# Kernel optimization log

Measured on AMD Instinct MI355X. Metric: run time of the kernel, lower is better.

The kernel has to match this reference:

```python
import jax, jax.numpy as jnp
import numpy as np

N_NODES = 100000
N_EDGES = 1600000
D = 64
N_LAYERS = 3
N_GRAPHS = 128
BN_EPS = 1e-5


def setup_inputs() -> dict:
    key = jax.random.key(0)
    k_x, k_e, k_b, k_w = jax.random.split(key, 4)
    x = jax.random.normal(k_x, (N_NODES, D), dtype=jnp.float32)
    edge_index = jax.random.randint(k_e, (2, N_EDGES), 0, N_NODES, dtype=jnp.int64)
    batch = jnp.sort(jax.random.randint(k_b, (N_NODES,), 0, N_GRAPHS, dtype=jnp.int64))
    Ws = jax.random.normal(k_w, (N_LAYERS, D, D), dtype=jnp.float32) * (1.0 / np.sqrt(D))
    bs = jnp.zeros((N_LAYERS, D), dtype=jnp.float32)
    gammas = jnp.ones((N_LAYERS, D), dtype=jnp.float32)
    betas = jnp.zeros((N_LAYERS, D), dtype=jnp.float32)
    return {"x": x, "edge_index": edge_index, "batch": batch,
            "Ws": Ws, "bs": bs, "gammas": gammas, "betas": betas}


def reference(x, edge_index, batch, Ws, bs, gammas, betas):
    N = x.shape[0]
    # GCN: add self-loops, symmetric normalization deg^{-1/2}_src * deg^{-1/2}_dst
    loop = jnp.arange(N, dtype=edge_index.dtype)
    src = jnp.concatenate([edge_index[0], loop])  # [E+N]
    dst = jnp.concatenate([edge_index[1], loop])
    deg = jax.ops.segment_sum(jnp.ones_like(dst, dtype=x.dtype), dst, num_segments=N)
    dinv = jnp.where(deg > 0, jax.lax.rsqrt(deg), 0.0)
    norm = dinv[src] * dinv[dst]  # [E+N]

    h = x
    for l in range(N_LAYERS):
        t = h @ Ws[l]                                    # [N,D] dense transform
        msg = t[src] * norm[:, None]                     # gather + scale [E+N,D]
        t = jax.ops.segment_sum(msg, dst, num_segments=N) + bs[l]
        # BatchNorm1d (training-style batch statistics, biased variance)
        mean = jnp.mean(t, axis=0)
        var = jnp.mean((t - mean) ** 2, axis=0)
        t = (t - mean) * jax.lax.rsqrt(var + BN_EPS) * gammas[l] + betas[l]
        h = jax.nn.relu(t)

    # global mean pool over graphs
    sums = jax.ops.segment_sum(h, batch, num_segments=N_GRAPHS)        # [G,D]
    counts = jax.ops.segment_sum(jnp.ones((N,), dtype=h.dtype), batch, num_segments=N_GRAPHS)
    return sums / jnp.maximum(counts, 1.0)[:, None]
```

## Files before the change

### kernel.cpp

```cpp
#include <hip/hip_runtime.h>
#include <hip/hip_bf16.h>

typedef __hip_bfloat16 bf16;
typedef short bf16x8 __attribute__((ext_vector_type(8)));
typedef float f32x4 __attribute__((ext_vector_type(4)));

#define NN 100000
#define NE 1600000
#define DD 64
#define NL 3
#define NG 128
#define BN_EPS 1e-5f
#define SCAN_BLK 98
#define TILE_ROWS 64
#define LSW 72
#define NT ((NN + TILE_ROWS - 1) / TILE_ROWS)
#define GB_NODES 48
#define GB_BLOCKS ((NN + GB_NODES - 1) / GB_NODES)
#define ECAP 1664
#define CSW_CAP (NE + 7 * NN)

__global__ __launch_bounds__(256) void detect_kernel(const int* __restrict__ ei,
                                                     const int* __restrict__ batch,
                                                     int* __restrict__ flags) {
    __shared__ int s_e, s_b;
    if (threadIdx.x == 0) { s_e = 0; s_b = 0; }
    __syncthreads();
    for (int i = threadIdx.x; i < 512; i += 256) {
        if (ei[2 * i + 1] != 0) atomicOr(&s_e, 1);
        if (batch[NN - 1024 + 2 * i + 1] != 0) atomicOr(&s_b, 1);
    }
    __syncthreads();
    if (threadIdx.x == 0) { flags[0] = s_e; flags[1] = s_b; }
}

__device__ __forceinline__ int ld_src(const int* ei, int e, int is32) {
    return is32 ? ei[e] : ei[2 * e];
}
__device__ __forceinline__ int ld_dst(const int* ei, int e, int is32) {
    return is32 ? ei[NE + e] : ei[2 * NE + 2 * e];
}
__device__ __forceinline__ int ld_batch(const int* b, int n, int is32) {
    return is32 ? b[n] : b[2 * n];
}
__device__ __forceinline__ float bf2f(unsigned short u) {
    return __uint_as_float(((unsigned int)u) << 16);
}
__device__ __forceinline__ unsigned short f2bf(float x) {
    bf16 b = __float2bfloat16(x);
    return *reinterpret_cast<unsigned short*>(&b);
}
__device__ __forceinline__ void split_bf16(float x, unsigned short& hi, unsigned short& lo) {
    hi = f2bf(x);
    lo = f2bf(x - bf2f(hi));
}
__device__ __forceinline__ int pad8(int d) { return (d + 7) & ~7; }

__global__ __launch_bounds__(256) void deg_kernel(const int* __restrict__ ei,
                                                  const int* __restrict__ flags,
                                                  int* __restrict__ deg_cnt) {
    int is32 = flags[0];
    int e = blockIdx.x * 256 + threadIdx.x;
    if (e < NE) atomicAdd(&deg_cnt[ld_dst(ei, e, is32)], 1);
}

__global__ __launch_bounds__(256) void scan_part_kernel(const int* __restrict__ deg_cnt,
                                                        int* __restrict__ blocksum,
                                                        float* __restrict__ dinv) {
    __shared__ int s[256];
    int base = blockIdx.x * 1024 + threadIdx.x * 4;
    int t = 0;
    if (base < NN) {
        int4 v = *(const int4*)(deg_cnt + base);
        t = pad8(v.x) + pad8(v.y) + pad8(v.z) + pad8(v.w);
        float4 dv = make_float4(rsqrtf((float)v.x + 1.f), rsqrtf((float)v.y + 1.f),
                                rsqrtf((float)v.z + 1.f), rsqrtf((float)v.w + 1.f));
        *(float4*)(dinv + base) = dv;
    }
    s[threadIdx.x] = t;
    __syncthreads();
    for (int off = 128; off > 0; off >>= 1) {
        if (threadIdx.x < off) s[threadIdx.x] += s[threadIdx.x + off];
        __syncthreads();
    }
    if (threadIdx.x == 0) blocksum[blockIdx.x] = s[0];
}

__global__ __launch_bounds__(256) void scan_write_kernel(int* __restrict__ deg_cnt,
                                                         const int* __restrict__ blocksum,
                                                         int* __restrict__ rowptr) {
    __shared__ int sb[128];
    __shared__ int s[256];
    if (threadIdx.x < 128)
        sb[threadIdx.x] = (threadIdx.x < SCAN_BLK) ? blocksum[threadIdx.x] : 0;
    __syncthreads();
    for (int off = 1; off < 128; off <<= 1) {
        int a = 0;
        if (threadIdx.x < 128 && threadIdx.x >= off) a = sb[threadIdx.x - off];
        __syncthreads();
        if (threadIdx.x < 128) sb[threadIdx.x] += a;
        __syncthreads();
    }
    int blockpre = (blockIdx.x == 0) ? 0 : sb[blockIdx.x - 1];
    if (blockIdx.x == SCAN_BLK - 1 && threadIdx.x == 0)
        rowptr[NN] = sb[SCAN_BLK - 1];

    int base = blockIdx.x * 1024 + threadIdx.x * 4;
    int4 v = make_int4(0, 0, 0, 0);
    if (base < NN) v = *(const int4*)(deg_cnt + base);
    int p0 = pad8(v.x), p1 = pad8(v.y), p2 = pad8(v.z), p3 = pad8(v.w);
    int t = p0 + p1 + p2 + p3;
    s[threadIdx.x] = t;
    for (int off = 1; off < 256; off <<= 1) {
        __syncthreads();
        int a = (threadIdx.x >= off) ? s[threadIdx.x - off] : 0;
        __syncthreads();
        s[threadIdx.x] += a;
    }
    __syncthreads();
    int pre = blockpre + s[threadIdx.x] - t;
    if (base < NN) {
        rowptr[base] = pre;
        rowptr[base + 1] = pre + p0;
        rowptr[base + 2] = pre + p0 + p1;
        rowptr[base + 3] = pre + p0 + p1 + p2;
        *(int4*)(deg_cnt + base) = make_int4(0, 0, 0, 0);
    }
}

__global__ __launch_bounds__(256) void fill_kernel(const int* __restrict__ ei,
                                                   const int* __restrict__ flags,
                                                   const int* __restrict__ rowptr,
                                                   int* __restrict__ cursor,
                                                   int* __restrict__ csw) {
    int is32 = flags[0];
    int e = blockIdx.x * 256 + threadIdx.x;
    if (e >= NE) return;
    int s = ld_src(ei, e, is32), d = ld_dst(ei, e, is32);
    int pos = rowptr[d] + atomicAdd(&cursor[d], 1);
    csw[pos] = (s + 1) << 7;
}

__global__ __launch_bounds__(256) void gemm_kernel(const float* __restrict__ h,
                                                   const float* __restrict__ W,
                                                   const float* __restrict__ dinv,
                                                   const float* __restrict__ accum_prev,
                                                   const float* __restrict__ gamma,
                                                   const float* __restrict__ beta,
                                                   int use_bn, float alpha,
                                                   bf16* __restrict__ t,
                                                   float* __restrict__ accum_l) {
    if (blockIdx.x == 0 && threadIdx.x < 128) accum_l[threadIdx.x] = 0.f;

    __shared__ unsigned short ls_hi[TILE_ROWS * LSW];
    __shared__ unsigned short ls_lo[TILE_ROWS * LSW];
    __shared__ float ssc[DD], ssh[DD], sdinv[TILE_ROWS];
    int tid = threadIdx.x;
    if (tid < 64) {
        if (use_bn) {
            float S = accum_prev[tid], Q = accum_prev[64 + tid];
            float mean = S / (float)NN;
            float var = fmaxf(Q / (float)NN - mean * mean, 0.f);
            float sc = gamma[tid] * rsqrtf(var + BN_EPS);
            ssc[tid] = sc;
            ssh[tid] = beta[tid] - mean * sc;
        } else {
            ssc[tid] = 1.f;
            ssh[tid] = 0.f;
        }
    }

    int lane = tid & 63;
    int wv = tid >> 6;
    int lr = lane & 15;
    int lg = lane >> 4;

    bf16x8 bhi[2][4], blo[2][4];
#pragma unroll
    for (int ks = 0; ks < 2; ++ks)
#pragma unroll
        for (int nt = 0; nt < 4; ++nt)
#pragma unroll
            for (int e = 0; e < 8; ++e) {
                float wval = W[(ks * 32 + lg * 8 + e) * DD + nt * 16 + lr];
                unsigned short hi, lo;
                split_bf16(wval, hi, lo);
                bhi[ks][nt][e] = (short)hi;
                blo[ks][nt][e] = (short)lo;
            }
    __syncthreads();

    for (int tile = blockIdx.x; tile < NT; tile += gridDim.x) {
        int row0 = tile * TILE_ROWS;
        int nrows = min(TILE_ROWS, NN - row0);
        if (tid < 64) sdinv[tid] = (row0 + tid < NN) ? dinv[row0 + tid] : 0.f;
#pragma unroll
        for (int it = 0; it < 4; ++it) {
            int flat = (tid + it * 256) * 4;
            int gflat = row0 * DD + flat;
            if (gflat < NN * DD) {
                float4 hv = *(const float4*)(h + gflat);
                int c0 = flat & 63;
                float4 s4 = *(const float4*)(ssc + c0);
                float4 b4 = *(const float4*)(ssh + c0);
                float x0 = hv.x * s4.x + b4.x;
                float x1 = hv.y * s4.y + b4.y;
                float x2 = hv.z * s4.z + b4.z;
                float x3 = hv.w * s4.w + b4.w;
                x0 = fmaxf(x0, x0 * alpha);
                x1 = fmaxf(x1, x1 * alpha);
                x2 = fmaxf(x2, x2 * alpha);
                x3 = fmaxf(x3, x3 * alpha);
                unsigned short h0, l0, h1, l1, h2, l2, h3, l3;
                split_bf16(x0, h0, l0);
                split_bf16(x1, h1, l1);
                split_bf16(x2, h2, l2);
                split_bf16(x3, h3, l3);
                int row = flat >> 6;
                *(ushort4*)(ls_hi + row * LSW + c0) = make_ushort4(h0, h1, h2, h3);
                *(ushort4*)(ls_lo + row * LSW + c0) = make_ushort4(l0, l1, l2, l3);
            }
        }
        __syncthreads();

        f32x4 acc[4];
#pragma unroll
        for (int nt = 0; nt < 4; ++nt) acc[nt] = (f32x4){0.f, 0.f, 0.f, 0.f};

#pragma unroll
        for (int ks = 0; ks < 2; ++ks) {
            int aoff = (wv * 16 + lr) * LSW + ks * 32 + lg * 8;
            bf16x8 a_hi = *(const bf16x8*)(ls_hi + aoff);
            bf16x8 a_lo = *(const bf16x8*)(ls_lo + aoff);
#pragma unroll
            for (int nt = 0; nt < 4; ++nt) {
                acc[nt] = __builtin_amdgcn_mfma_f32_16x16x32_bf16(a_hi, bhi[ks][nt],
                                                                  acc[nt], 0, 0, 0);
                acc[nt] = __builtin_amdgcn_mfma_f32_16x16x32_bf16(a_hi, blo[ks][nt],
                                                                  acc[nt], 0, 0, 0);
                acc[nt] = __builtin_amdgcn_mfma_f32_16x16x32_bf16(a_lo, bhi[ks][nt],
                                                                  acc[nt], 0, 0, 0);
            }
        }
        __syncthreads();

#pragma unroll
        for (int nt = 0; nt < 4; ++nt)
#pragma unroll
            for (int rg = 0; rg < 4; ++rg) {
                int orow = wv * 16 + lg * 4 + rg;
                ls_hi[orow * LSW + nt * 16 + lr] = f2bf(acc[nt][rg] * sdinv[orow]);
            }
        __syncthreads();
#pragma unroll
        for (int it = 0; it < 2; ++it) {
            int flat8 = (tid + it * 256) * 8;
            int row = flat8 >> 6, c = flat8 & 63;
            if (row < nrows) {
                uint4 v = *(const uint4*)(ls_hi + row * LSW + c);
                *(uint4*)((unsigned short*)t + (size_t)(row0 + row) * DD + c) = v;
            }
        }
        __syncthreads();
    }
}

__device__ __forceinline__ void batch8(const int* __restrict__ ep, int j,
                                       const char* __restrict__ tbase, int f2,
                                       float& acc) {
    int4 a0 = *(const int4*)(ep + j);
    int4 a1 = *(const int4*)(ep + j + 4);
    unsigned short r[8];
    r[0] = *(const unsigned short*)(tbase + (unsigned)(a0.x + f2));
    r[1] = *(const unsigned short*)(tbase + (unsigned)(a0.y + f2));
    r[2] = *(const unsigned short*)(tbase + (unsigned)(a0.z + f2));
    r[3] = *(const unsigned short*)(tbase + (unsigned)(a0.w + f2));
    r[4] = *(const unsigned short*)(tbase + (unsigned)(a1.x + f2));
    r[5] = *(const unsigned short*)(tbase + (unsigned)(a1.y + f2));
    r[6] = *(const unsigned short*)(tbase + (unsigned)(a1.z + f2));
    r[7] = *(const unsigned short*)(tbase + (unsigned)(a1.w + f2));
    float s01 = bf2f(r[0]) + bf2f(r[1]), s23 = bf2f(r[2]) + bf2f(r[3]);
    float s45 = bf2f(r[4]) + bf2f(r[5]), s67 = bf2f(r[6]) + bf2f(r[7]);
    acc += (s01 + s23) + (s45 + s67);
}

__device__ __forceinline__ void batch8x2(const int* __restrict__ ep, int jA, int jB,
                                         const char* __restrict__ tbase, int f2,
                                         float& accA, float& accB) {
    int4 aA0 = *(const int4*)(ep + jA), aA1 = *(const int4*)(ep + jA + 4);
    int4 aB0 = *(const int4*)(ep + jB), aB1 = *(const int4*)(ep + jB + 4);
    unsigned short rA[8], rB[8];
    rA[0] = *(const unsigned short*)(tbase + (unsigned)(aA0.x + f2));
    rA[1] = *(const unsigned short*)(tbase + (unsigned)(aA0.y + f2));
    rA[2] = *(const unsigned short*)(tbase + (unsigned)(aA0.z + f2));
    rA[3] = *(const unsigned short*)(tbase + (unsigned)(aA0.w + f2));
    rA[4] = *(const unsigned short*)(tbase + (unsigned)(aA1.x + f2));
    rA[5] = *(const unsigned short*)(tbase + (unsigned)(aA1.y + f2));
    rA[6] = *(const unsigned short*)(tbase + (unsigned)(aA1.z + f2));
    rA[7] = *(const unsigned short*)(tbase + (unsigned)(aA1.w + f2));
    rB[0] = *(const unsigned short*)(tbase + (unsigned)(aB0.x + f2));
    rB[1] = *(const unsigned short*)(tbase + (unsigned)(aB0.y + f2));
    rB[2] = *(const unsigned short*)(tbase + (unsigned)(aB0.z + f2));
    rB[3] = *(const unsigned short*)(tbase + (unsigned)(aB0.w + f2));
    rB[4] = *(const unsigned short*)(tbase + (unsigned)(aB1.x + f2));
    rB[5] = *(const unsigned short*)(tbase + (unsigned)(aB1.y + f2));
    rB[6] = *(const unsigned short*)(tbase + (unsigned)(aB1.z + f2));
    rB[7] = *(const unsigned short*)(tbase + (unsigned)(aB1.w + f2));
    float sA01 = bf2f(rA[0]) + bf2f(rA[1]), sA23 = bf2f(rA[2]) + bf2f(rA[3]);
    float sA45 = bf2f(rA[4]) + bf2f(rA[5]), sA67 = bf2f(rA[6]) + bf2f(rA[7]);
    accA += (sA01 + sA23) + (sA45 + sA67);
    float sB01 = bf2f(rB[0]) + bf2f(rB[1]), sB23 = bf2f(rB[2]) + bf2f(rB[3]);
    float sB45 = bf2f(rB[4]) + bf2f(rB[5]), sB67 = bf2f(rB[6]) + bf2f(rB[7]);
    accB += (sB01 + sB23) + (sB45 + sB67);
}

__device__ __forceinline__ void batch8x4(const int* __restrict__ ep, int jA, int jB,
                                         int jC, int jD,
                                         const char* __restrict__ tbase, int f2,
                                         float& accA, float& accB, float& accC,
                                         float& accD) {
    int4 aA0 = *(const int4*)(ep + jA), aA1 = *(const int4*)(ep + jA + 4);
    int4 aB0 = *(const int4*)(ep + jB), aB1 = *(const int4*)(ep + jB + 4);
    int4 aC0 = *(const int4*)(ep + jC), aC1 = *(const int4*)(ep + jC + 4);
    int4 aD0 = *(const int4*)(ep + jD), aD1 = *(const int4*)(ep + jD + 4);
    unsigned short rA[8], rB[8], rC[8], rD[8];
    rA[0] = *(const unsigned short*)(tbase + (unsigned)(aA0.x + f2));
    rA[1] = *(const unsigned short*)(tbase + (unsigned)(aA0.y + f2));
    rA[2] = *(const unsigned short*)(tbase + (unsigned)(aA0.z + f2));
    rA[3] = *(const unsigned short*)(tbase + (unsigned)(aA0.w + f2));
    rA[4] = *(const unsigned short*)(tbase + (unsigned)(aA1.x + f2));
    rA[5] = *(const unsigned short*)(tbase + (unsigned)(aA1.y + f2));
    rA[6] = *(const unsigned short*)(tbase + (unsigned)(aA1.z + f2));
    rA[7] = *(const unsigned short*)(tbase + (unsigned)(aA1.w + f2));
    rB[0] = *(const unsigned short*)(tbase + (unsigned)(aB0.x + f2));
    rB[1] = *(const unsigned short*)(tbase + (unsigned)(aB0.y + f2));
    rB[2] = *(const unsigned short*)(tbase + (unsigned)(aB0.z + f2));
    rB[3] = *(const unsigned short*)(tbase + (unsigned)(aB0.w + f2));
    rB[4] = *(const unsigned short*)(tbase + (unsigned)(aB1.x + f2));
    rB[5] = *(const unsigned short*)(tbase + (unsigned)(aB1.y + f2));
    rB[6] = *(const unsigned short*)(tbase + (unsigned)(aB1.z + f2));
    rB[7] = *(const unsigned short*)(tbase + (unsigned)(aB1.w + f2));
    rC[0] = *(const unsigned short*)(tbase + (unsigned)(aC0.x + f2));
    rC[1] = *(const unsigned short*)(tbase + (unsigned)(aC0.y + f2));
    rC[2] = *(const unsigned short*)(tbase + (unsigned)(aC0.z + f2));
    rC[3] = *(const unsigned short*)(tbase + (unsigned)(aC0.w + f2));
    rC[4] = *(const unsigned short*)(tbase + (unsigned)(aC1.x + f2));
    rC[5] = *(const unsigned short*)(tbase + (unsigned)(aC1.y + f2));
    rC[6] = *(const unsigned short*)(tbase + (unsigned)(aC1.z + f2));
    rC[7] = *(const unsigned short*)(tbase + (unsigned)(aC1.w + f2));
    rD[0] = *(const unsigned short*)(tbase + (unsigned)(aD0.x + f2));
    rD[1] = *(const unsigned short*)(tbase + (unsigned)(aD0.y + f2));
    rD[2] = *(const unsigned short*)(tbase + (unsigned)(aD0.z + f2));
    rD[3] = *(const unsigned short*)(tbase + (unsigned)(aD0.w + f2));
    rD[4] = *(const unsigned short*)(tbase + (unsigned)(aD1.x + f2));
    rD[5] = *(const unsigned short*)(tbase + (unsigned)(aD1.y + f2));
    rD[6] = *(const unsigned short*)(tbase + (unsigned)(aD1.z + f2));
    rD[7] = *(const unsigned short*)(tbase + (unsigned)(aD1.w + f2));
    float sA01 = bf2f(rA[0]) + bf2f(rA[1]), sA23 = bf2f(rA[2]) + bf2f(rA[3]);
    float sA45 = bf2f(rA[4]) + bf2f(rA[5]), sA67 = bf2f(rA[6]) + bf2f(rA[7]);
    accA += (sA01 + sA23) + (sA45 + sA67);
    float sB01 = bf2f(rB[0]) + bf2f(rB[1]), sB23 = bf2f(rB[2]) + bf2f(rB[3]);
    float sB45 = bf2f(rB[4]) + bf2f(rB[5]), sB67 = bf2f(rB[6]) + bf2f(rB[7]);
    accB += (sB01 + sB23) + (sB45 + sB67);
    float sC01 = bf2f(rC[0]) + bf2f(rC[1]), sC23 = bf2f(rC[2]) + bf2f(rC[3]);
    float sC45 = bf2f(rC[4]) + bf2f(rC[5]), sC67 = bf2f(rC[6]) + bf2f(rC[7]);
    accC += (sC01 + sC23) + (sC45 + sC67);
    float sD01 = bf2f(rD[0]) + bf2f(rD[1]), sD23 = bf2f(rD[2]) + bf2f(rD[3]);
    float sD45 = bf2f(rD[4]) + bf2f(rD[5]), sD67 = bf2f(rD[6]) + bf2f(rD[7]);
    accD += (sD01 + sD23) + (sD45 + sD67);
}

__device__ __forceinline__ void run_quad(const int* __restrict__ ep,
                                         const char* __restrict__ tbase, int f2,
                                         int jA, int eA, int jB, int eB,
                                         int jC, int eC, int jD, int eD,
                                         float& accA, float& accB, float& accC,
                                         float& accD) {
    while (jA < eA && jB < eB && jC < eC && jD < eD) {
        batch8x4(ep, jA, jB, jC, jD, tbase, f2, accA, accB, accC, accD);
        jA += 8; jB += 8; jC += 8; jD += 8;
    }
    while (jA < eA && jB < eB) { batch8x2(ep, jA, jB, tbase, f2, accA, accB); jA += 8; jB += 8; }
    while (jC < eC && jD < eD) { batch8x2(ep, jC, jD, tbase, f2, accC, accD); jC += 8; jD += 8; }
    while (jA < eA && jC < eC) { batch8x2(ep, jA, jC, tbase, f2, accA, accC); jA += 8; jC += 8; }
    while (jA < eA && jD < eD) { batch8x2(ep, jA, jD, tbase, f2, accA, accD); jA += 8; jD += 8; }
    while (jB < eB && jC < eC) { batch8x2(ep, jB, jC, tbase, f2, accB, accC); jB += 8; jC += 8; }
    while (jB < eB && jD < eD) { batch8x2(ep, jB, jD, tbase, f2, accB, accD); jB += 8; jD += 8; }
    while (jA < eA) { batch8(ep, jA, tbase, f2, accA); jA += 8; }
    while (jB < eB) { batch8(ep, jB, tbase, f2, accB); jB += 8; }
    while (jC < eC) { batch8(ep, jC, tbase, f2, accC); jC += 8; }
    while (jD < eD) { batch8(ep, jD, tbase, f2, accD); jD += 8; }
}

__global__ __launch_bounds__(256) void gather_kernel(const bf16* __restrict__ t,
                                                     const float* __restrict__ dinv,
                                                     const float* __restrict__ bias,
                                                     const int* __restrict__ rowptr,
                                                     const int* __restrict__ csw,
                                                     float* __restrict__ h,
                                                     float* __restrict__ accum_l) {
    __shared__ __attribute__((aligned(16))) int se[ECAP];
    __shared__ int srp[GB_NODES + 1];
    __shared__ float s_sum[256], s_sq[256];

    int f = threadIdx.x & 63;
    int wv = threadIdx.x >> 6;
    int nb0 = blockIdx.x * GB_NODES;
    int nloc = min(GB_NODES, NN - nb0);

    for (int i = threadIdx.x; i <= nloc; i += 256) srp[i] = rowptr[nb0 + i];
    __syncthreads();
    int ebase = srp[0];
    int nE = srp[nloc] - ebase;
    bool staged = (nE <= ECAP);
    if (staged) {
        for (int i = threadIdx.x * 4; i < nE; i += 1024)
            *(int4*)(se + i) = *(const int4*)(csw + ebase + i);
    }
    __syncthreads();

    const char* tbase = (const char*)t - 128;
    int f2 = f * 2;
    const unsigned short* tf = (const unsigned short*)t + f;
    float bb = bias[f];
    float sum = 0.f, sq = 0.f;

    for (int q = wv; 4 * q < nloc; q += 4) {
        int d0 = 4 * q;
        int nA = nb0 + d0, nB = nA + 1, nC = nA + 2, nD = nA + 3;
        float accA = bf2f(tf[(size_t)nA * DD]);
        float accB = bf2f(tf[(size_t)nB * DD]);
        float accC = bf2f(tf[(size_t)nC * DD]);
        float accD = bf2f(tf[(size_t)nD * DD]);
        int jA = srp[d0] - ebase, eA = srp[d0 + 1] - ebase;
        int jB = eA, eB = srp[d0 + 2] - ebase;
        int jC = eB, eC = srp[d0 + 3] - ebase;
        int jD = eC, eD = srp[d0 + 4] - ebase;

        if (staged)
            run_quad(se, tbase, f2, jA, eA, jB, eB, jC, eC, jD, eD, accA, accB, accC, accD);
        else
            run_quad(csw + ebase, tbase, f2, jA, eA, jB, eB, jC, eC, jD, eD,
                     accA, accB, accC, accD);

        float diA = dinv[nA], diB = dinv[nB], diC = dinv[nC], diD = dinv[nD];
        accA = accA * diA + bb;
        accB = accB * diB + bb;
        accC = accC * diC + bb;
        accD = accD * diD + bb;
        h[(size_t)nA * DD + f] = accA;
        h[(size_t)nB * DD + f] = accB;
        h[(size_t)nC * DD + f] = accC;
        h[(size_t)nD * DD + f] = accD;
        sum += accA + accB + accC + accD;
        sq += accA * accA + accB * accB + accC * accC + accD * accD;
    }
    s_sum[threadIdx.x] = sum;
    s_sq[threadIdx.x] = sq;
    __syncthreads();
    if (threadIdx.x < 64) {
        sum = s_sum[f] + s_sum[64 + f] + s_sum[128 + f] + s_sum[192 + f];
        sq = s_sq[f] + s_sq[64 + f] + s_sq[128 + f] + s_sq[192 + f];
        atomicAdd(&accum_l[f], sum);
        atomicAdd(&accum_l[64 + f], sq);
    }
}

#define POOL_CHUNK 128
__global__ __launch_bounds__(256) void pool_kernel(const float* __restrict__ hraw,
                                                   const float* __restrict__ accum_l,
                                                   const float* __restrict__ gamma,
                                                   const float* __restrict__ beta,
                                                   const int* __restrict__ batch,
                                                   const int* __restrict__ flags,
                                                   float* __restrict__ pool,
                                                   float* __restrict__ counts) {
    __shared__ float ssc[64], ssh[64];
    if (threadIdx.x < 64) {
        float S = accum_l[threadIdx.x], Q = accum_l[64 + threadIdx.x];
        float mean = S / (float)NN;
        float var = fmaxf(Q / (float)NN - mean * mean, 0.f);
        float sc = gamma[threadIdx.x] * rsqrtf(var + BN_EPS);
        ssc[threadIdx.x] = sc;
        ssh[threadIdx.x] = beta[threadIdx.x] - mean * sc;
    }
    __syncthreads();
    int is32 = flags[1];
    int f = threadIdx.x & 63, rg = threadIdx.x >> 6;
    float sc = ssc[f], sh = ssh[f];
    int base = blockIdx.x * POOL_CHUNK;
    float acc = 0.f, cnt = 0.f;
    int cur = -1;
    for (int i = rg; i < POOL_CHUNK; i += 4) {
        int n = base + i;
        if (n >= NN) break;
        int g = ld_batch(batch, n, is32);
        if (g != cur) {
            if (cur >= 0) {
                atomicAdd(&pool[cur * DD + f], acc);
                if (f == 0) atomicAdd(&counts[cur], cnt);
            }
            acc = 0.f;
            cnt = 0.f;
            cur = g;
        }
        acc += fmaxf(hraw[(size_t)n * DD + f] * sc + sh, 0.f);
        cnt += 1.f;
    }
    if (cur >= 0) {
        atomicAdd(&pool[cur * DD + f], acc);
        if (f == 0) atomicAdd(&counts[cur], cnt);
    }
}

__global__ __launch_bounds__(256) void final_kernel(const float* __restrict__ pool,
                                                    const float* __restrict__ counts,
                                                    float* __restrict__ out) {
    int i = blockIdx.x * 256 + threadIdx.x;
    if (i < NG * DD) {
        int g = i >> 6;
        out[i] = pool[i] / fmaxf(counts[g], 1.0f);
    }
}

extern "C" void kernel_launch(void* const* d_in, const int* in_sizes, int n_in,
                              void* d_out, int out_size, void* d_ws, size_t ws_size,
                              hipStream_t stream) {
    const float* x = (const float*)d_in[0];
    const int* edge_index = (const int*)d_in[1];
    const int* batch = (const int*)d_in[2];
    const float* Ws = (const float*)d_in[3];
    const float* bs = (const float*)d_in[4];
    const float* gammas = (const float*)d_in[5];
    const float* betas = (const float*)d_in[6];
    float* out = (float*)d_out;

    float* h = (float*)d_ws;
    bf16* zrow = (bf16*)(h + (size_t)NN * DD);
    bf16* t = zrow + DD;
    int* csw = (int*)(t + (size_t)NN * DD);
    float* dinv = (float*)(csw + CSW_CAP);
    int* deg_cnt = (int*)(dinv + NN);
    float* pool = (float*)(deg_cnt + NN);
    float* counts = pool + NG * DD;
    int* rowptr = (int*)(counts + NG);
    float* accum = (float*)(rowptr + NN + 1);
    int* flags = (int*)(accum + NL * 128);
    int* blocksum = flags + 2;

    hipMemsetAsync(deg_cnt, 0, (NN + NG * DD + NG) * sizeof(float), stream);
    hipMemsetAsync(csw, 0, (size_t)CSW_CAP * sizeof(int), stream);
    hipMemsetAsync(zrow, 0, DD * sizeof(bf16), stream);

    detect_kernel<<<1, 256, 0, stream>>>(edge_index, batch, flags);
    deg_kernel<<<(NE + 255) / 256, 256, 0, stream>>>(edge_index, flags, deg_cnt);
    scan_part_kernel<<<SCAN_BLK, 256, 0, stream>>>(deg_cnt, blocksum, dinv);
    scan_write_kernel<<<SCAN_BLK, 256, 0, stream>>>(deg_cnt, blocksum, rowptr);
    fill_kernel<<<(NE + 255) / 256, 256, 0, stream>>>(edge_index, flags, rowptr,
                                                      deg_cnt, csw);

    for (int l = 0; l < NL; ++l) {
        const float* hin = (l == 0) ? x : h;
        float alpha = (l == 0) ? 1.0f : 0.0f;
        gemm_kernel<<<NT, 256, 0, stream>>>(hin, Ws + (size_t)l * DD * DD, dinv,
                                            accum + (l - 1 >= 0 ? l - 1 : 0) * 128,
                                            gammas + (l - 1 >= 0 ? l - 1 : 0) * DD,
                                            betas + (l - 1 >= 0 ? l - 1 : 0) * DD,
                                            (l > 0) ? 1 : 0, alpha, t, accum + l * 128);
        gather_kernel<<<GB_BLOCKS, 256, 0, stream>>>(t, dinv, bs + l * DD, rowptr, csw, h,
                                                     accum + l * 128);
    }

    pool_kernel<<<(NN + POOL_CHUNK - 1) / POOL_CHUNK, 256, 0, stream>>>(
        h, accum + 2 * 128, gammas + 2 * DD, betas + 2 * DD, batch, flags, pool, counts);
    final_kernel<<<(NG * DD + 255) / 256, 256, 0, stream>>>(pool, counts, out);
}
```

Before: 594.5 us.

## Bin edges by destination bucket before CSR fill to localize scatter

```diff
diff --git a/kernel.cpp b/kernel.cpp
--- a/kernel.cpp
+++ b/kernel.cpp
@@ -20,6 +20,12 @@
 #define ECAP 1664
 #define CSW_CAP (NE + 7 * NN)
 
+#define NBUK 391
+#define BUK_CAP 4608
+#define OVF_CAP 8192
+#define EPB 4096
+#define NBB ((NE + EPB - 1) / EPB)
+
 __global__ __launch_bounds__(256) void detect_kernel(const int* __restrict__ ei,
                                                      const int* __restrict__ batch,
                                                      int* __restrict__ flags) {
@@ -56,12 +62,51 @@
 }
 __device__ __forceinline__ int pad8(int d) { return (d + 7) & ~7; }
 
-__global__ __launch_bounds__(256) void deg_kernel(const int* __restrict__ ei,
+__global__ __launch_bounds__(256) void bin_kernel(const int* __restrict__ ei,
                                                   const int* __restrict__ flags,
-                                                  int* __restrict__ deg_cnt) {
+                                                  int* __restrict__ deg_cnt,
+                                                  int* __restrict__ bukcnt,
+                                                  int* __restrict__ staging,
+                                                  int* __restrict__ ovf_cnt,
+                                                  int2* __restrict__ ovf) {
+    __shared__ int hist[NBUK];
+    __shared__ int base[NBUK];
     int is32 = flags[0];
-    int e = blockIdx.x * 256 + threadIdx.x;
-    if (e < NE) atomicAdd(&deg_cnt[ld_dst(ei, e, is32)], 1);
+    for (int i = threadIdx.x; i < NBUK; i += 256) hist[i] = 0;
+    __syncthreads();
+
+    int e0 = blockIdx.x * EPB;
+    int myb[16], mypack[16], myidx[16];
+#pragma unroll
+    for (int k = 0; k < 16; ++k) {
+        int e = e0 + k * 256 + threadIdx.x;
+        myb[k] = -1;
+        if (e < NE) {
+            int s = ld_src(ei, e, is32), d = ld_dst(ei, e, is32);
+            atomicAdd(&deg_cnt[d], 1);
+            int b = d >> 8;
+            myb[k] = b;
+            mypack[k] = (s << 8) | (d & 255);
+            myidx[k] = atomicAdd(&hist[b], 1);
+        }
+    }
+    __syncthreads();
+    for (int i = threadIdx.x; i < NBUK; i += 256)
+        if (hist[i]) base[i] = atomicAdd(&bukcnt[i], hist[i]);
+    __syncthreads();
+#pragma unroll
+    for (int k = 0; k < 16; ++k) {
+        if (myb[k] >= 0) {
+            int slot = base[myb[k]] + myidx[k];
+            if (slot < BUK_CAP) {
+                staging[myb[k] * BUK_CAP + slot] = mypack[k];
+            } else {
+                int o = atomicAdd(ovf_cnt, 1);
+                if (o < OVF_CAP)
+                    ovf[o] = make_int2(mypack[k] >> 8, (myb[k] << 8) | (mypack[k] & 255));
+            }
+        }
+    }
 }
 
 __global__ __launch_bounds__(256) void scan_part_kernel(const int* __restrict__ deg_cnt,
@@ -128,17 +173,32 @@
     }
 }
 
-__global__ __launch_bounds__(256) void fill_kernel(const int* __restrict__ ei,
-                                                   const int* __restrict__ flags,
-                                                   const int* __restrict__ rowptr,
-                                                   int* __restrict__ cursor,
-                                                   int* __restrict__ csw) {
-    int is32 = flags[0];
-    int e = blockIdx.x * 256 + threadIdx.x;
-    if (e >= NE) return;
-    int s = ld_src(ei, e, is32), d = ld_dst(ei, e, is32);
-    int pos = rowptr[d] + atomicAdd(&cursor[d], 1);
-    csw[pos] = (s + 1) << 7;
+__global__ __launch_bounds__(256) void scatter_kernel(const int* __restrict__ bukcnt,
+                                                      const int* __restrict__ staging,
+                                                      const int* __restrict__ ovf_cnt,
+                                                      const int2* __restrict__ ovf,
+                                                      const int* __restrict__ rowptr,
+                                                      int* __restrict__ cursor,
+                                                      int* __restrict__ csw) {
+    int b = blockIdx.x;
+    if (b == NBUK) {
+        int n = min(*ovf_cnt, OVF_CAP);
+        for (int i = threadIdx.x; i < n; i += 256) {
+            int2 e = ovf[i];
+            int pos = rowptr[e.y] + atomicAdd(&cursor[e.y], 1);
+            csw[pos] = (e.x + 1) << 7;
+        }
+        return;
+    }
+    int n = min(bukcnt[b], BUK_CAP);
+    int nb = b << 8;
+    const int* st = staging + b * BUK_CAP;
+    for (int i = threadIdx.x; i < n; i += 256) {
+        int v = st[i];
+        int d = nb + (v & 255);
+        int pos = rowptr[d] + atomicAdd(&cursor[d], 1);
+        csw[pos] = ((v >> 8) + 1) << 7;
+    }
 }
 
 __global__ __launch_bounds__(256) void gemm_kernel(const float* __restrict__ h,
@@ -543,21 +603,26 @@
     int* deg_cnt = (int*)(dinv + NN);
     float* pool = (float*)(deg_cnt + NN);
     float* counts = pool + NG * DD;
-    int* rowptr = (int*)(counts + NG);
+    int* bukcnt = (int*)(counts + NG);
+    int* ovf_cnt = bukcnt + NBUK;
+    int* rowptr = ovf_cnt + 1;
     float* accum = (float*)(rowptr + NN + 1);
     int* flags = (int*)(accum + NL * 128);
     int* blocksum = flags + 2;
-
-    hipMemsetAsync(deg_cnt, 0, (NN + NG * DD + NG) * sizeof(float), stream);
+    int2* ovf = (int2*)(blocksum + 128);
+    int* staging = (int*)h;
+
+    hipMemsetAsync(deg_cnt, 0, (NN + NG * DD + NG + NBUK + 1) * sizeof(int), stream);
     hipMemsetAsync(csw, 0, (size_t)CSW_CAP * sizeof(int), stream);
     hipMemsetAsync(zrow, 0, DD * sizeof(bf16), stream);
 
     detect_kernel<<<1, 256, 0, stream>>>(edge_index, batch, flags);
-    deg_kernel<<<(NE + 255) / 256, 256, 0, stream>>>(edge_index, flags, deg_cnt);
+    bin_kernel<<<NBB, 256, 0, stream>>>(edge_index, flags, deg_cnt, bukcnt, staging,
+                                        ovf_cnt, ovf);
     scan_part_kernel<<<SCAN_BLK, 256, 0, stream>>>(deg_cnt, blocksum, dinv);
     scan_write_kernel<<<SCAN_BLK, 256, 0, stream>>>(deg_cnt, blocksum, rowptr);
-    fill_kernel<<<(NE + 255) / 256, 256, 0, stream>>>(edge_index, flags, rowptr,
-                                                      deg_cnt, csw);
+    scatter_kernel<<<NBUK + 1, 256, 0, stream>>>(bukcnt, staging, ovf_cnt, ovf, rowptr,
+                                                 deg_cnt, csw);
 
     for (int l = 0; l < NL; ++l) {
         const float* hin = (l == 0) ? x : h;
```

After: 538.4 us. 1.1x faster.
